# Performance work log

Measured on AMD Instinct MI355X. Metric: run time of the kernel, lower is better.

Reference implementation:

```python
import jax, jax.numpy as jnp
import numpy as np

T, G, K, N = 8192, 8, 1024, 2048

def setup_inputs() -> dict:
    key = jax.random.key(0)
    k1, k2, k3 = jax.random.split(key, 3)
    x = jax.random.normal(k1, (T, K), dtype=jnp.float32)
    w = jax.random.normal(k2, (G, N, K), dtype=jnp.float32) * 0.02
    # cumulative end-offsets per group: sorted, last entry == T (covers all tokens)
    offs = jnp.sort(jax.random.randint(k3, (G,), 0, T).astype(jnp.int32))
    offs = offs.at[-1].set(T)
    return {"input": x, "weight": w, "grouped_mm_offs": offs}

def reference(input, weight, grouped_mm_offs):
    # grouped_mm(input, weight.transpose(1,2), offs): token t in group g iff
    # offs[g-1] <= t < offs[g]; out[t] = input[t] @ weight[g].T
    t = input.shape[0]
    g = weight.shape[0]
    gid = jnp.searchsorted(grouped_mm_offs, jnp.arange(t), side="right")  # [T]
    out = jnp.zeros((t, weight.shape[1]), dtype=input.dtype)
    for gi in range(g):  # fixed small expert loop; data dims stay vectorized
        xg = jnp.where((gid == gi)[:, None], input, jnp.zeros((), input.dtype))
        out = out + xg @ weight[gi].T
    return out
```

## Files before the change

kernel.cpp:

```cpp
#include <hip/hip_runtime.h>
#include <hip/hip_bf16.h>


#define T_DIM 8192
#define G_DIM 8
#define K_DIM 1024
#define N_DIM 2048

using short8  = __attribute__((ext_vector_type(8))) short;
using f32x4   = __attribute__((ext_vector_type(4))) float;
using ushort8 = __attribute__((ext_vector_type(8))) unsigned short;

typedef __attribute__((address_space(1))) void gvoid;
typedef __attribute__((address_space(3))) void lvoid;

__global__ __launch_bounds__(256) void cvt_kernel(const float* __restrict__ x,
                                                  const float* __restrict__ w,
                                                  ushort8* __restrict__ xb,
                                                  ushort8* __restrict__ wb,
                                                  int n8x, int n8tot) {
  int i = blockIdx.x * blockDim.x + threadIdx.x;
  if (i >= n8tot) return;
  const float4* s; ushort8* d; int j;
  if (i < n8x) { s = (const float4*)x; d = xb; j = i; }
  else         { s = (const float4*)w; d = wb; j = i - n8x; }
  float4 v0 = s[2 * j], v1 = s[2 * j + 1];
  ushort8 o;
  o[0] = __builtin_bit_cast(unsigned short, __float2bfloat16(v0.x));
  o[1] = __builtin_bit_cast(unsigned short, __float2bfloat16(v0.y));
  o[2] = __builtin_bit_cast(unsigned short, __float2bfloat16(v0.z));
  o[3] = __builtin_bit_cast(unsigned short, __float2bfloat16(v0.w));
  o[4] = __builtin_bit_cast(unsigned short, __float2bfloat16(v1.x));
  o[5] = __builtin_bit_cast(unsigned short, __float2bfloat16(v1.y));
  o[6] = __builtin_bit_cast(unsigned short, __float2bfloat16(v1.z));
  o[7] = __builtin_bit_cast(unsigned short, __float2bfloat16(v1.w));
  d[j] = o;
}

__global__ __launch_bounds__(256) void grouped_gemm_kernel(
    const __hip_bfloat16* __restrict__ xb,
    const __hip_bfloat16* __restrict__ wb,
    const int* __restrict__ offs,
    float* __restrict__ out) {
  const int g  = blockIdx.z;
  const int m0 = blockIdx.y * 128;
  const int n0 = blockIdx.x * 128;
  const int lo = g ? offs[g - 1] : 0;
  const int hi = offs[g];
  if (lo >= m0 + 128 || hi <= m0 || hi <= lo) return;

  __shared__ __align__(16) __hip_bfloat16 As[128 * 64];
  __shared__ __align__(16) __hip_bfloat16 Bs[128 * 64];

  const __hip_bfloat16* wg = wb + (size_t)g * N_DIM * K_DIM;

  const int lane = threadIdx.x & 63;
  const int wid  = threadIdx.x >> 6;
  const int wm   = wid >> 1;
  const int wn   = wid & 1;

  const int srow = lane >> 3;
  const int scol = ((lane & 7) ^ srow) * 8;

  f32x4 acc[4][4] = {};

  for (int kk = 0; kk < K_DIM / 64; ++kk) {
    const int k0 = kk * 64;
#pragma unroll
    for (int i = 0; i < 4; ++i) {
      const int j   = wid * 4 + i;
      const int row = j * 8 + srow;
      const __hip_bfloat16* ga = xb + (size_t)(m0 + row) * K_DIM + k0 + scol;
      const __hip_bfloat16* gb = wg + (size_t)(n0 + row) * K_DIM + k0 + scol;
      __builtin_amdgcn_global_load_lds((gvoid*)ga, (lvoid*)(As + j * 512), 16, 0, 0);
      __builtin_amdgcn_global_load_lds((gvoid*)gb, (lvoid*)(Bs + j * 512), 16, 0, 0);
    }
    __syncthreads();

#pragma unroll
    for (int ks = 0; ks < 2; ++ks) {
      const int kb  = ks * 4 + (lane >> 4);
      const int off = ((kb ^ (lane & 7)) * 8);
      short8 a[4], b[4];
#pragma unroll
      for (int mt = 0; mt < 4; ++mt)
        a[mt] = *reinterpret_cast<const short8*>(
            As + (wm * 64 + mt * 16 + (lane & 15)) * 64 + off);
#pragma unroll
      for (int nt = 0; nt < 4; ++nt)
        b[nt] = *reinterpret_cast<const short8*>(
            Bs + (wn * 64 + nt * 16 + (lane & 15)) * 64 + off);
#pragma unroll
      for (int mt = 0; mt < 4; ++mt)
#pragma unroll
        for (int nt = 0; nt < 4; ++nt)
          acc[mt][nt] = __builtin_amdgcn_mfma_f32_16x16x32_bf16(
              a[mt], b[nt], acc[mt][nt], 0, 0, 0);
    }
    __syncthreads();
  }

  const int quad = lane >> 4;
#pragma unroll
  for (int mt = 0; mt < 4; ++mt) {
    const int rbase = m0 + wm * 64 + mt * 16 + quad * 4;
#pragma unroll
    for (int r = 0; r < 4; ++r) {
      const int row = rbase + r;
      if (row < lo || row >= hi) continue;
#pragma unroll
      for (int nt = 0; nt < 4; ++nt) {
        const int col = n0 + wn * 64 + nt * 16 + (lane & 15);
        out[(size_t)row * N_DIM + col] = acc[mt][nt][r];
      }
    }
  }
}

__global__ __launch_bounds__(256) void fallback_kernel(
    const float* __restrict__ x, const float* __restrict__ w,
    const int* __restrict__ offs, float* __restrict__ out) {
  __shared__ float xs[K_DIM];
  const int t = blockIdx.y;
  int g = 0;
  while (g < G_DIM - 1 && offs[g] <= t) ++g;
  for (int i = threadIdx.x; i < K_DIM; i += blockDim.x)
    xs[i] = x[(size_t)t * K_DIM + i];
  __syncthreads();
  const int n = blockIdx.x * blockDim.x + threadIdx.x;
  const float* wr = w + ((size_t)g * N_DIM + n) * K_DIM;
  float s = 0.f;
  for (int k = 0; k < K_DIM; ++k) s += xs[k] * wr[k];
  out[(size_t)t * N_DIM + n] = s;
}

extern "C" void kernel_launch(void* const* d_in, const int* in_sizes, int n_in,
                              void* d_out, int out_size, void* d_ws, size_t ws_size,
                              hipStream_t stream) {
  const float* x    = (const float*)d_in[0];
  const float* w    = (const float*)d_in[1];
  const int*   offs = (const int*)d_in[2];
  float*       out  = (float*)d_out;

  const size_t x_elems = (size_t)T_DIM * K_DIM;
  const size_t w_elems = (size_t)G_DIM * N_DIM * K_DIM;
  const size_t need    = (x_elems + w_elems) * sizeof(__hip_bfloat16);

  if (ws_size < need) {
    fallback_kernel<<<dim3(N_DIM / 256, T_DIM), 256, 0, stream>>>(x, w, offs, out);
    return;
  }

  __hip_bfloat16* xb = (__hip_bfloat16*)d_ws;
  __hip_bfloat16* wb = xb + x_elems;

  const int n8x   = (int)(x_elems / 8);
  const int n8tot = (int)((x_elems + w_elems) / 8);
  cvt_kernel<<<(n8tot + 255) / 256, 256, 0, stream>>>(
      x, w, (ushort8*)xb, (ushort8*)wb, n8x, n8tot);

  grouped_gemm_kernel<<<dim3(N_DIM / 128, T_DIM / 128, G_DIM), 256, 0, stream>>>(
      xb, wb, offs, out);
}
```

Baseline: 191.3 us.

## Fuse fp32-to-bf16 conversion into grouped GEMM with register-prefetched tile loads

Drops the separate conversion kernel. The GEMM now loads fp32 x and w tiles straight into registers, converts them to bf16 and writes them swizzled into LDS. The next k-tile is prefetched into registers while the current tile is computed, which removes the extra launch and the bf16 workspace round trip. In exchange, each block re-reads fp32 data at twice the bytes, and any weight tile shared across m-blocks is converted many times over. Register pressure rises, and the fallback path is removed.

```diff
diff --git a/kernel.cpp b/kernel.cpp
--- a/kernel.cpp
+++ b/kernel.cpp
@@ -7,41 +7,30 @@
 #define K_DIM 1024
 #define N_DIM 2048
 
-using short8  = __attribute__((ext_vector_type(8))) short;
-using f32x4   = __attribute__((ext_vector_type(4))) float;
-using ushort8 = __attribute__((ext_vector_type(8))) unsigned short;
+using short8 = __attribute__((ext_vector_type(8))) short;
+using f32x4  = __attribute__((ext_vector_type(4))) float;
 
-typedef __attribute__((address_space(1))) void gvoid;
-typedef __attribute__((address_space(3))) void lvoid;
+__device__ __forceinline__ void barrier_lgkm() {
+  asm volatile("s_waitcnt lgkmcnt(0)\n\ts_barrier" ::: "memory");
+}
 
-__global__ __launch_bounds__(256) void cvt_kernel(const float* __restrict__ x,
-                                                  const float* __restrict__ w,
-                                                  ushort8* __restrict__ xb,
-                                                  ushort8* __restrict__ wb,
-                                                  int n8x, int n8tot) {
-  int i = blockIdx.x * blockDim.x + threadIdx.x;
-  if (i >= n8tot) return;
-  const float4* s; ushort8* d; int j;
-  if (i < n8x) { s = (const float4*)x; d = xb; j = i; }
-  else         { s = (const float4*)w; d = wb; j = i - n8x; }
-  float4 v0 = s[2 * j], v1 = s[2 * j + 1];
-  ushort8 o;
-  o[0] = __builtin_bit_cast(unsigned short, __float2bfloat16(v0.x));
-  o[1] = __builtin_bit_cast(unsigned short, __float2bfloat16(v0.y));
-  o[2] = __builtin_bit_cast(unsigned short, __float2bfloat16(v0.z));
-  o[3] = __builtin_bit_cast(unsigned short, __float2bfloat16(v0.w));
-  o[4] = __builtin_bit_cast(unsigned short, __float2bfloat16(v1.x));
-  o[5] = __builtin_bit_cast(unsigned short, __float2bfloat16(v1.y));
-  o[6] = __builtin_bit_cast(unsigned short, __float2bfloat16(v1.z));
-  o[7] = __builtin_bit_cast(unsigned short, __float2bfloat16(v1.w));
-  d[j] = o;
+__device__ __forceinline__ short8 cvt8(float4 u, float4 v) {
+  float2 f0{u.x, u.y}, f1{u.z, u.w}, f2{v.x, v.y}, f3{v.z, v.w};
+  __hip_bfloat162 p0 = __float22bfloat162_rn(f0);
+  __hip_bfloat162 p1 = __float22bfloat162_rn(f1);
+  __hip_bfloat162 p2 = __float22bfloat162_rn(f2);
+  __hip_bfloat162 p3 = __float22bfloat162_rn(f3);
+  short8 o;
+  o[0] = __builtin_bit_cast(short, p0.x); o[1] = __builtin_bit_cast(short, p0.y);
+  o[2] = __builtin_bit_cast(short, p1.x); o[3] = __builtin_bit_cast(short, p1.y);
+  o[4] = __builtin_bit_cast(short, p2.x); o[5] = __builtin_bit_cast(short, p2.y);
+  o[6] = __builtin_bit_cast(short, p3.x); o[7] = __builtin_bit_cast(short, p3.y);
+  return o;
 }
 
 __global__ __launch_bounds__(256) void grouped_gemm_kernel(
-    const __hip_bfloat16* __restrict__ xb,
-    const __hip_bfloat16* __restrict__ wb,
-    const int* __restrict__ offs,
-    float* __restrict__ out) {
+    const float* __restrict__ x, const float* __restrict__ w,
+    const int* __restrict__ offs, float* __restrict__ out) {
   const int g  = blockIdx.z;
   const int m0 = blockIdx.y * 128;
   const int n0 = blockIdx.x * 128;
@@ -52,44 +41,56 @@
   __shared__ __align__(16) __hip_bfloat16 As[128 * 64];
   __shared__ __align__(16) __hip_bfloat16 Bs[128 * 64];
 
-  const __hip_bfloat16* wg = wb + (size_t)g * N_DIM * K_DIM;
+  const float* wg = w + (size_t)g * N_DIM * K_DIM;
 
-  const int lane = threadIdx.x & 63;
-  const int wid  = threadIdx.x >> 6;
+  const int tid  = threadIdx.x;
+  const int lane = tid & 63;
+  const int wid  = tid >> 6;
   const int wm   = wid >> 1;
   const int wn   = wid & 1;
 
-  const int srow = lane >> 3;
-  const int scol = ((lane & 7) ^ srow) * 8;
+  const int r0    = tid >> 3;
+  const int kb    = tid & 7;
+  const int swoff = ((kb ^ (r0 & 7)) * 8);
+  const float* ax = x  + (size_t)(m0 + r0) * K_DIM + kb * 8;
+  const float* bw = wg + (size_t)(n0 + r0) * K_DIM + kb * 8;
+
+  float4 av[4][2], bv[4][2];
+  auto load_tiles = [&](int k0) {
+#pragma unroll
+    for (int c = 0; c < 4; ++c) {
+      const float* pa = ax + (size_t)(32 * c) * K_DIM + k0;
+      const float* pb = bw + (size_t)(32 * c) * K_DIM + k0;
+      av[c][0] = *(const float4*)(pa);
+      av[c][1] = *(const float4*)(pa + 4);
+      bv[c][0] = *(const float4*)(pb);
+      bv[c][1] = *(const float4*)(pb + 4);
+    }
+  };
 
   f32x4 acc[4][4] = {};
+  load_tiles(0);
 
   for (int kk = 0; kk < K_DIM / 64; ++kk) {
-    const int k0 = kk * 64;
 #pragma unroll
-    for (int i = 0; i < 4; ++i) {
-      const int j   = wid * 4 + i;
-      const int row = j * 8 + srow;
-      const __hip_bfloat16* ga = xb + (size_t)(m0 + row) * K_DIM + k0 + scol;
-      const __hip_bfloat16* gb = wg + (size_t)(n0 + row) * K_DIM + k0 + scol;
-      __builtin_amdgcn_global_load_lds((gvoid*)ga, (lvoid*)(As + j * 512), 16, 0, 0);
-      __builtin_amdgcn_global_load_lds((gvoid*)gb, (lvoid*)(Bs + j * 512), 16, 0, 0);
+    for (int c = 0; c < 4; ++c) {
+      *(short8*)(As + (r0 + 32 * c) * 64 + swoff) = cvt8(av[c][0], av[c][1]);
+      *(short8*)(Bs + (r0 + 32 * c) * 64 + swoff) = cvt8(bv[c][0], bv[c][1]);
     }
-    __syncthreads();
+    if (kk + 1 < K_DIM / 64) load_tiles((kk + 1) * 64);
+    barrier_lgkm();
 
 #pragma unroll
     for (int ks = 0; ks < 2; ++ks) {
-      const int kb  = ks * 4 + (lane >> 4);
-      const int off = ((kb ^ (lane & 7)) * 8);
+      const int kbf = ks * 4 + (lane >> 4);
+      const int off = ((kbf ^ (lane & 7)) * 8);
       short8 a[4], b[4];
 #pragma unroll
       for (int mt = 0; mt < 4; ++mt)
-        a[mt] = *reinterpret_cast<const short8*>(
-            As + (wm * 64 + mt * 16 + (lane & 15)) * 64 + off);
+        a[mt] = *(const short8*)(As + (wm * 64 + mt * 16 + (lane & 15)) * 64 + off);
 #pragma unroll
       for (int nt = 0; nt < 4; ++nt)
-        b[nt] = *reinterpret_cast<const short8*>(
-            Bs + (wn * 64 + nt * 16 + (lane & 15)) * 64 + off);
+        b[nt] = *(const short8*)(Bs + (wn * 64 + nt * 16 + (lane & 15)) * 64 + off);
 #pragma unroll
       for (int mt = 0; mt < 4; ++mt)
 #pragma unroll
@@ -97,7 +98,7 @@
           acc[mt][nt] = __builtin_amdgcn_mfma_f32_16x16x32_bf16(
               a[mt], b[nt], acc[mt][nt], 0, 0, 0);
     }
-    __syncthreads();
+    barrier_lgkm();
   }
 
   const int quad = lane >> 4;
@@ -117,23 +118,6 @@
   }
 }
 
-__global__ __launch_bounds__(256) void fallback_kernel(
-    const float* __restrict__ x, const float* __restrict__ w,
-    const int* __restrict__ offs, float* __restrict__ out) {
-  __shared__ float xs[K_DIM];
-  const int t = blockIdx.y;
-  int g = 0;
-  while (g < G_DIM - 1 && offs[g] <= t) ++g;
-  for (int i = threadIdx.x; i < K_DIM; i += blockDim.x)
-    xs[i] = x[(size_t)t * K_DIM + i];
-  __syncthreads();
-  const int n = blockIdx.x * blockDim.x + threadIdx.x;
-  const float* wr = w + ((size_t)g * N_DIM + n) * K_DIM;
-  float s = 0.f;
-  for (int k = 0; k < K_DIM; ++k) s += xs[k] * wr[k];
-  out[(size_t)t * N_DIM + n] = s;
-}
-
 extern "C" void kernel_launch(void* const* d_in, const int* in_sizes, int n_in,
                               void* d_out, int out_size, void* d_ws, size_t ws_size,
                               hipStream_t stream) {
@@ -141,24 +125,8 @@
   const float* w    = (const float*)d_in[1];
   const int*   offs = (const int*)d_in[2];
   float*       out  = (float*)d_out;
-
-  const size_t x_elems = (size_t)T_DIM * K_DIM;
-  const size_t w_elems = (size_t)G_DIM * N_DIM * K_DIM;
-  const size_t need    = (x_elems + w_elems) * sizeof(__hip_bfloat16);
-
-  if (ws_size < need) {
-    fallback_kernel<<<dim3(N_DIM / 256, T_DIM), 256, 0, stream>>>(x, w, offs, out);
-    return;
-  }
-
-  __hip_bfloat16* xb = (__hip_bfloat16*)d_ws;
-  __hip_bfloat16* wb = xb + x_elems;
-
-  const int n8x   = (int)(x_elems / 8);
-  const int n8tot = (int)((x_elems + w_elems) / 8);
-  cvt_kernel<<<(n8tot + 255) / 256, 256, 0, stream>>>(
-      x, w, (ushort8*)xb, (ushort8*)wb, n8x, n8tot);
+  (void)d_ws; (void)ws_size; (void)in_sizes; (void)n_in; (void)out_size;
 
   grouped_gemm_kernel<<<dim3(N_DIM / 128, T_DIM / 128, G_DIM), 256, 0, stream>>>(
-      xb, wb, offs, out);
+      x, w, offs, out);
 }
```

New measurement: 223.4 us. 1.17x slower.

## Compact grouped GEMM grid to active group-tile pairs and grid-stride conversion

Applied to the files above, without the earlier changes.

The GEMM grid is changed from a dense (N-tiles, M-tiles, groups) launch, where most blocks exit immediately, to a compact list of at most 72 (group, M-tile) pairs computed in-kernel from the offsets, with an occupancy hint of 4 waves per SIMD. The fp32-to-bf16 conversion kernel becomes a fixed 4096-block grid-stride loop using nontemporal loads, unrolled by two. This removes the launch and scheduling cost of roughly 7/8 empty blocks, at the price of a per-block prefix scan over the offsets. MAX_PAIRS=72 assumes at most 64 tiles plus 8 partial boundary tiles.

```diff
diff --git a/kernel.cpp b/kernel.cpp
--- a/kernel.cpp
+++ b/kernel.cpp
@@ -6,6 +6,7 @@
 #define G_DIM 8
 #define K_DIM 1024
 #define N_DIM 2048
+#define MAX_PAIRS 72
 
 using short8  = __attribute__((ext_vector_type(8))) short;
 using f32x4   = __attribute__((ext_vector_type(4))) float;
@@ -19,35 +20,55 @@
                                                   ushort8* __restrict__ xb,
                                                   ushort8* __restrict__ wb,
                                                   int n8x, int n8tot) {
-  int i = blockIdx.x * blockDim.x + threadIdx.x;
-  if (i >= n8tot) return;
-  const float4* s; ushort8* d; int j;
-  if (i < n8x) { s = (const float4*)x; d = xb; j = i; }
-  else         { s = (const float4*)w; d = wb; j = i - n8x; }
-  float4 v0 = s[2 * j], v1 = s[2 * j + 1];
-  ushort8 o;
-  o[0] = __builtin_bit_cast(unsigned short, __float2bfloat16(v0.x));
-  o[1] = __builtin_bit_cast(unsigned short, __float2bfloat16(v0.y));
-  o[2] = __builtin_bit_cast(unsigned short, __float2bfloat16(v0.z));
-  o[3] = __builtin_bit_cast(unsigned short, __float2bfloat16(v0.w));
-  o[4] = __builtin_bit_cast(unsigned short, __float2bfloat16(v1.x));
-  o[5] = __builtin_bit_cast(unsigned short, __float2bfloat16(v1.y));
-  o[6] = __builtin_bit_cast(unsigned short, __float2bfloat16(v1.z));
-  o[7] = __builtin_bit_cast(unsigned short, __float2bfloat16(v1.w));
-  d[j] = o;
+  const int stride = gridDim.x * blockDim.x;
+  for (int i = blockIdx.x * blockDim.x + threadIdx.x; i < n8tot; i += 2 * stride) {
+#pragma unroll
+    for (int u = 0; u < 2; ++u) {
+      const int idx = i + u * stride;
+      if (idx >= n8tot) break;
+      const f32x4* s; ushort8* d; int j;
+      if (idx < n8x) { s = (const f32x4*)x; d = xb; j = idx; }
+      else           { s = (const f32x4*)w; d = wb; j = idx - n8x; }
+      f32x4 v0 = __builtin_nontemporal_load(&s[2 * j]);
+      f32x4 v1 = __builtin_nontemporal_load(&s[2 * j + 1]);
+      ushort8 o;
+      o[0] = __builtin_bit_cast(unsigned short, __float2bfloat16(v0[0]));
+      o[1] = __builtin_bit_cast(unsigned short, __float2bfloat16(v0[1]));
+      o[2] = __builtin_bit_cast(unsigned short, __float2bfloat16(v0[2]));
+      o[3] = __builtin_bit_cast(unsigned short, __float2bfloat16(v0[3]));
+      o[4] = __builtin_bit_cast(unsigned short, __float2bfloat16(v1[0]));
+      o[5] = __builtin_bit_cast(unsigned short, __float2bfloat16(v1[1]));
+      o[6] = __builtin_bit_cast(unsigned short, __float2bfloat16(v1[2]));
+      o[7] = __builtin_bit_cast(unsigned short, __float2bfloat16(v1[3]));
+      d[j] = o;
+    }
+  }
 }
 
-__global__ __launch_bounds__(256) void grouped_gemm_kernel(
+__global__ __launch_bounds__(256, 4) void grouped_gemm_kernel(
     const __hip_bfloat16* __restrict__ xb,
     const __hip_bfloat16* __restrict__ wb,
     const int* __restrict__ offs,
     float* __restrict__ out) {
-  const int g  = blockIdx.z;
-  const int m0 = blockIdx.y * 128;
+  int offv[G_DIM];
+#pragma unroll
+  for (int i = 0; i < G_DIM; ++i) offv[i] = offs[i];
+
+  const int p = blockIdx.y;
+  int g = -1, tile = 0, lo = 0, hi = 0, pre = 0;
+#pragma unroll
+  for (int gi = 0; gi < G_DIM; ++gi) {
+    const int l = gi ? offv[gi - 1] : 0;
+    const int h = offv[gi];
+    const int t0 = l >> 7;
+    const int cnt = (h > l) ? (((h + 127) >> 7) - t0) : 0;
+    if (g < 0 && p < pre + cnt) { g = gi; tile = t0 + (p - pre); lo = l; hi = h; }
+    pre += cnt;
+  }
+  if (g < 0) return;
+
+  const int m0 = tile * 128;
   const int n0 = blockIdx.x * 128;
-  const int lo = g ? offs[g - 1] : 0;
-  const int hi = offs[g];
-  if (lo >= m0 + 128 || hi <= m0 || hi <= lo) return;
 
   __shared__ __align__(16) __hip_bfloat16 As[128 * 64];
   __shared__ __align__(16) __hip_bfloat16 Bs[128 * 64];
@@ -156,9 +177,9 @@
 
   const int n8x   = (int)(x_elems / 8);
   const int n8tot = (int)((x_elems + w_elems) / 8);
-  cvt_kernel<<<(n8tot + 255) / 256, 256, 0, stream>>>(
-      x, w, (ushort8*)xb, (ushort8*)wb, n8x, n8tot);
+  cvt_kernel<<<4096, 256, 0, stream>>>(x, w, (ushort8*)xb, (ushort8*)wb,
+                                       n8x, n8tot);
 
-  grouped_gemm_kernel<<<dim3(N_DIM / 128, T_DIM / 128, G_DIM), 256, 0, stream>>>(
+  grouped_gemm_kernel<<<dim3(N_DIM / 128, MAX_PAIRS), 256, 0, stream>>>(
       xb, wb, offs, out);
 }
```

New measurement: 184.0 us. 1.04x faster.
